# Kernel optimization log

Hardware: AMD Instinct MI355X
Metric: run time of the kernel (lower is better)

Reference implementation:

```python
import jax, jax.numpy as jnp
import numpy as np


def _greedy_nms_single(scores, suppress):
    """Greedy score-ordered suppression for one scene.
    scores: [P] float max class score; suppress: [P, P] bool, row i suppresses col j
    (same class AND within class radius of point i). Returns keep mask [P] bool."""
    P = scores.shape[0]

    def cond(state):
        alive, _ = state
        return jnp.any(alive)

    def body(state):
        alive, keep = state
        i = jnp.argmax(jnp.where(alive, scores, -jnp.inf))  # highest-score remaining
        keep = keep.at[i].set(True)
        alive = alive & ~suppress[i]   # drop same-class points within radius of i
        alive = alive.at[i].set(False)
        return alive, keep

    alive0 = jnp.ones((P,), dtype=bool)
    keep0 = jnp.zeros((P,), dtype=bool)
    _, keep = jax.lax.while_loop(cond, body, (alive0, keep0))
    return keep


def _keep_mask(centers, cls_preds, class_radius):
    # centers: [B,P,3], cls_preds: [B,P,K], class_radius: [K]
    scores = jnp.max(cls_preds, axis=-1)     # [B,P]  torch.max(..., dim=1) values
    labels = jnp.argmax(cls_preds, axis=-1)  # [B,P]  torch.max(..., dim=1) indices
    diff = centers[:, :, None, :] - centers[:, None, :, :]        # [B,P,P,3]
    dist = jnp.sqrt(jnp.sum(diff * diff, axis=-1))                # [B,P,P] torch.norm
    same_class = labels[:, :, None] == labels[:, None, :]         # [B,P,P]
    radii = class_radius[labels]                                  # [B,P] radius of keeper i
    suppress = same_class & (dist < radii[:, :, None])            # [B,P,P]
    return jax.vmap(_greedy_nms_single)(scores, suppress)         # [B,P] bool


def setup_inputs() -> dict:
    key = jax.random.key(0)
    k1, k2, k3, k4 = jax.random.split(key, 4)
    B, P, C, K = 8, 2048, 1024, 3
    centers = jax.random.normal(k1, (B, P, 3), dtype=jnp.float32)
    features = jax.random.normal(k2, (B, P, C), dtype=jnp.float32)
    cls_preds = jax.random.normal(k3, (B, P, K), dtype=jnp.float32)
    class_radius = jax.random.uniform(k4, (K,), dtype=jnp.float32)  # per-class NMS radius
    return {"centers": centers, "features": features, "cls_preds": cls_preds,
            "class_radius": class_radius}


def reference(centers, features, cls_preds, class_radius):
    """Greedy per-class radius-based keypoint suppression (fixed-shape variant):
    instead of dynamically gathering kept points (data-dependent shape), we return
    the boolean keep mask and the inputs with suppressed entries zeroed out."""
    keep = _keep_mask(centers, cls_preds, class_radius)      # [B,P] bool
    m = keep[..., None].astype(features.dtype)
    return (centers * m, features * m, cls_preds * m, keep)
```

## Files before the change

kernel.cpp:

```cpp
#include <hip/hip_runtime.h>

#define B 8
#define P 2048
#define C 1024
#define NCHUNK 32
#define FEAT4 (B*P*C/4)
#define CEN4  (B*P*3/4)

typedef unsigned long long u64;
typedef unsigned int u32;

__device__ __forceinline__ u64 shfl_xor_u64(u64 x, int m) {
    int lo = __shfl_xor((int)(u32)x, m, 64);
    int hi = __shfl_xor((int)(u32)(x >> 32), m, 64);
    return ((u64)(u32)hi << 32) | (u32)lo;
}

__global__ __launch_bounds__(1024) void sort_kernel(
    const float* __restrict__ centers,
    const float* __restrict__ cls_preds,
    float4* __restrict__ scent,
    int* __restrict__ sidx)
{
    __shared__ u64 s_k[P];
    const int b = blockIdx.x, tid = threadIdx.x;
    const float* clsb = cls_preds + (size_t)b * P * 3;
    const float* cenb = centers + (size_t)b * P * 3;

    u64 v[2];
    #pragma unroll
    for (int h = 0; h < 2; ++h) {
        int e = tid + h * 1024;
        float s0 = clsb[e*3], s1 = clsb[e*3+1], s2 = clsb[e*3+2];
        float sc = s0; int lb = 0;
        if (s1 > sc) { sc = s1; lb = 1; }
        if (s2 > sc) { sc = s2; lb = 2; }
        u32 ub = __float_as_uint(sc);
        u32 ord = (ub & 0x80000000u) ? ~ub : (ub | 0x80000000u);
        v[h] = ((u64)(~ord) << 32) | (u32)((e << 2) | lb);
    }
    for (int k = 2; k <= P; k <<= 1) {
        for (int j = k >> 1; j >= 64; j >>= 1) {
            s_k[tid] = v[0]; s_k[tid + 1024] = v[1];
            __syncthreads();
            #pragma unroll
            for (int h = 0; h < 2; ++h) {
                int e = tid + h * 1024;
                u64 p = s_k[e ^ j];
                bool asc = (e & k) == 0, upper = (e & j) != 0;
                u64 mn = v[h] < p ? v[h] : p, mx = v[h] < p ? p : v[h];
                v[h] = (asc != upper) ? mn : mx;
            }
            __syncthreads();
        }
        int jt = (k >> 1) < 32 ? (k >> 1) : 32;
        for (int j = jt; j >= 1; j >>= 1) {
            #pragma unroll
            for (int h = 0; h < 2; ++h) {
                int e = tid + h * 1024;
                u64 p = shfl_xor_u64(v[h], j);
                bool asc = (e & k) == 0, upper = (e & j) != 0;
                u64 mn = v[h] < p ? v[h] : p, mx = v[h] < p ? p : v[h];
                v[h] = (asc != upper) ? mn : mx;
            }
        }
    }
    s_k[tid] = v[0]; s_k[tid + 1024] = v[1];
    __syncthreads();
    #pragma unroll
    for (int h = 0; h < 2; ++h) {
        int pos = tid + h * 1024;
        u32 lo = (u32)s_k[pos];
        int orig = (int)(lo >> 2);
        float4 c;
        c.x = cenb[orig*3]; c.y = cenb[orig*3+1]; c.z = cenb[orig*3+2];
        c.w = __int_as_float((int)(lo & 3));
        scent[b * P + pos] = c;
        sidx[b * P + pos] = (int)lo;
    }
}

__global__ __launch_bounds__(512) void matrix_kernel(
    const float4* __restrict__ scent,
    const float* __restrict__ class_radius,
    u32* __restrict__ matT)
{
    __shared__ float4 s_cent[P];
    const int b = blockIdx.x >> 5, gi = blockIdx.x & 31;
    const int tid = threadIdx.x, wv = tid >> 6, lane = tid & 63;

    const float4 cj = scent[(size_t)b * P + (gi << 6) + lane];
    const int labj = __float_as_int(cj.w);
    const float r = class_radius[labj];
    const float r2 = r * r;

    for (int i = tid; i < P; i += 512) s_cent[i] = scent[(size_t)b * P + i];
    __syncthreads();

    for (int w = wv; w < 64; w += 8) {
        u32 acc = 0;
        #pragma unroll
        for (int u = 0; u < 32; ++u) {
            float4 ci = s_cent[(w << 5) + u];
            float dx = cj.x - ci.x, dy = cj.y - ci.y, dz = cj.z - ci.z;
            bool sup = (__float_as_int(ci.w) == labj)
                       && (dx*dx + dy*dy + dz*dz < r2);
            acc |= ((u32)sup) << u;
        }
        matT[((size_t)b * 64 + w) * P + (gi << 6) + lane] = acc;
    }
}

__global__ __launch_bounds__(576) void scan_kernel(
    const u32* __restrict__ matT,
    const int* __restrict__ sidx,
    float* __restrict__ out_keep)
{
    __shared__ u32 s_tile[2][64][65];
    __shared__ u32 s_removed[64];
    __shared__ int s_sidx[P];
    const int b = blockIdx.x;
    const int tid = threadIdx.x, wv = tid >> 6, lane = tid & 63;
    const u32* mb = matT + (size_t)b * 64 * P;

    for (int i = tid; i < P; i += 576) s_sidx[i] = sidx[(size_t)b * P + i];
    if (tid < 64) s_removed[tid] = 0;
    if (wv >= 1) {
        #pragma unroll
        for (int rr = 0; rr < 8; ++rr) {
            int w = ((wv - 1) << 3) + rr;
            s_tile[0][lane][w] = mb[(size_t)w * P + lane];
        }
    }
    __syncthreads();

    for (int g = 0; g < NCHUNK; ++g) {
        const int buf = g & 1;
        if (wv >= 1 && g + 1 < NCHUNK) {
            const int nb = (g + 1) << 6;
            #pragma unroll
            for (int rr = 0; rr < 8; ++rr) {
                int w = ((wv - 1) << 3) + rr;
                s_tile[buf ^ 1][lane][w] = mb[(size_t)w * P + nb + lane];
            }
        }
        if (wv == 0) {
            const int base = g << 6;
            u64 row = (u64)s_tile[buf][lane][2*g]
                    | ((u64)s_tile[buf][lane][2*g + 1] << 32);
            u64 rem = (u64)s_removed[2*g] | ((u64)s_removed[2*g + 1] << 32);
            u64 alive = ~rem;
            const u64 below = (1ull << lane) - 1ull;
            u64 keepm = 0;
            while (alive) {
                bool ok = ((alive >> lane) & 1ull) && ((row & alive & below) == 0ull);
                u64 newk = __ballot(ok);
                keepm |= newk;
                bool dead = (row & newk) != 0ull;
                u64 deadm = __ballot(dead);
                alive &= ~(newk | deadm);
            }
            int orig = s_sidx[base + lane] >> 2;
            out_keep[(size_t)b * P + orig] = ((keepm >> lane) & 1ull) ? 1.0f : 0.0f;
            u32 acc = 0;
            u64 m = keepm;
            while (m) {
                int q = (int)__ffsll((long long)m) - 1;
                acc |= s_tile[buf][q][lane];
                m &= m - 1ull;
            }
            s_removed[lane] |= acc;
        }
        __syncthreads();
    }
}

__global__ __launch_bounds__(256) void mask_kernel(
    const float* __restrict__ centers,
    const float* __restrict__ features,
    const float* __restrict__ cls_preds,
    const float* __restrict__ keep,
    float* __restrict__ out_centers,
    float* __restrict__ out_feat,
    float* __restrict__ out_cls)
{
    const int idx = blockIdx.x * 256 + threadIdx.x;
    if (idx < FEAT4) {
        const int row = idx >> 8;
        const float m = keep[row];
        float4 v = ((const float4*)features)[idx];
        v.x *= m; v.y *= m; v.z *= m; v.w *= m;
        ((float4*)out_feat)[idx] = v;
    } else if (idx < FEAT4 + CEN4) {
        const int q = idx - FEAT4;
        float4 v = ((const float4*)centers)[q];
        const int e = q * 4;
        v.x *= keep[(e    ) / 3]; v.y *= keep[(e + 1) / 3];
        v.z *= keep[(e + 2) / 3]; v.w *= keep[(e + 3) / 3];
        ((float4*)out_centers)[q] = v;
    } else if (idx < FEAT4 + 2 * CEN4) {
        const int q = idx - FEAT4 - CEN4;
        float4 v = ((const float4*)cls_preds)[q];
        const int e = q * 4;
        v.x *= keep[(e    ) / 3]; v.y *= keep[(e + 1) / 3];
        v.z *= keep[(e + 2) / 3]; v.w *= keep[(e + 3) / 3];
        ((float4*)out_cls)[q] = v;
    }
}

extern "C" void kernel_launch(void* const* d_in, const int* in_sizes, int n_in,
                              void* d_out, int out_size, void* d_ws, size_t ws_size,
                              hipStream_t stream) {
    const float* centers      = (const float*)d_in[0];
    const float* features     = (const float*)d_in[1];
    const float* cls_preds    = (const float*)d_in[2];
    const float* class_radius = (const float*)d_in[3];

    float* out = (float*)d_out;
    float* out_centers = out;
    float* out_feat    = out + (size_t)B * P * 3;
    float* out_cls     = out_feat + (size_t)B * P * C;
    float* out_keep    = out_cls + (size_t)B * P * 3;

    u32*    matT  = (u32*)out_feat;
    float4* scent = (float4*)(out_feat + 1048576);
    int*    sidx  = (int*)(out_feat + 1048576 + 65536);

    hipLaunchKernelGGL(sort_kernel, dim3(B), dim3(1024), 0, stream,
                       centers, cls_preds, scent, sidx);
    hipLaunchKernelGGL(matrix_kernel, dim3(B * 32), dim3(512), 0, stream,
                       scent, class_radius, matT);
    hipLaunchKernelGGL(scan_kernel, dim3(B), dim3(576), 0, stream,
                       matT, sidx, out_keep);
    hipLaunchKernelGGL(mask_kernel, dim3((FEAT4 + 2 * CEN4 + 255) / 256), dim3(256),
                       0, stream,
                       centers, features, cls_preds, out_keep,
                       out_centers, out_feat, out_cls);
}
```

Measured before the change: 191.9 us.

## Replace per-batch bitonic sort with parallel rank-counting sort across many blocks

Swaps the single-block-per-scene bitonic sort for a rank sort: each of 256 blocks rebuilds the full key array for its scene in shared memory and computes exact ranks for 64 keys by counting smaller keys, split across 8 waves. This spreads the sort over many more CUs and removes the long chain of barrier-separated bitonic stages. In exchange it does O(P^2) comparisons and recomputes keys redundantly in every block. Keys are unique because they embed the index, so ranks form a valid permutation.

```diff
diff --git a/kernel.cpp b/kernel.cpp
--- a/kernel.cpp
+++ b/kernel.cpp
@@ -10,73 +10,50 @@
 typedef unsigned long long u64;
 typedef unsigned int u32;
 
-__device__ __forceinline__ u64 shfl_xor_u64(u64 x, int m) {
-    int lo = __shfl_xor((int)(u32)x, m, 64);
-    int hi = __shfl_xor((int)(u32)(x >> 32), m, 64);
-    return ((u64)(u32)hi << 32) | (u32)lo;
-}
-
-__global__ __launch_bounds__(1024) void sort_kernel(
+__global__ __launch_bounds__(512) void rank_kernel(
     const float* __restrict__ centers,
     const float* __restrict__ cls_preds,
     float4* __restrict__ scent,
     int* __restrict__ sidx)
 {
-    __shared__ u64 s_k[P];
-    const int b = blockIdx.x, tid = threadIdx.x;
+    __shared__ u64 s_keys[P];
+    __shared__ u32 s_cnt[64][9];
+    const int b = blockIdx.x >> 5, gi = blockIdx.x & 31;
+    const int tid = threadIdx.x, wv = tid >> 6, lane = tid & 63;
     const float* clsb = cls_preds + (size_t)b * P * 3;
     const float* cenb = centers + (size_t)b * P * 3;
 
-    u64 v[2];
-    #pragma unroll
-    for (int h = 0; h < 2; ++h) {
-        int e = tid + h * 1024;
+    for (int e = tid; e < P; e += 512) {
         float s0 = clsb[e*3], s1 = clsb[e*3+1], s2 = clsb[e*3+2];
         float sc = s0; int lb = 0;
         if (s1 > sc) { sc = s1; lb = 1; }
         if (s2 > sc) { sc = s2; lb = 2; }
         u32 ub = __float_as_uint(sc);
         u32 ord = (ub & 0x80000000u) ? ~ub : (ub | 0x80000000u);
-        v[h] = ((u64)(~ord) << 32) | (u32)((e << 2) | lb);
-    }
-    for (int k = 2; k <= P; k <<= 1) {
-        for (int j = k >> 1; j >= 64; j >>= 1) {
-            s_k[tid] = v[0]; s_k[tid + 1024] = v[1];
-            __syncthreads();
-            #pragma unroll
-            for (int h = 0; h < 2; ++h) {
-                int e = tid + h * 1024;
-                u64 p = s_k[e ^ j];
-                bool asc = (e & k) == 0, upper = (e & j) != 0;
-                u64 mn = v[h] < p ? v[h] : p, mx = v[h] < p ? p : v[h];
-                v[h] = (asc != upper) ? mn : mx;
-            }
-            __syncthreads();
-        }
-        int jt = (k >> 1) < 32 ? (k >> 1) : 32;
-        for (int j = jt; j >= 1; j >>= 1) {
-            #pragma unroll
-            for (int h = 0; h < 2; ++h) {
-                int e = tid + h * 1024;
-                u64 p = shfl_xor_u64(v[h], j);
-                bool asc = (e & k) == 0, upper = (e & j) != 0;
-                u64 mn = v[h] < p ? v[h] : p, mx = v[h] < p ? p : v[h];
-                v[h] = (asc != upper) ? mn : mx;
-            }
-        }
-    }
-    s_k[tid] = v[0]; s_k[tid + 1024] = v[1];
-    __syncthreads();
-    #pragma unroll
-    for (int h = 0; h < 2; ++h) {
-        int pos = tid + h * 1024;
-        u32 lo = (u32)s_k[pos];
+        s_keys[e] = ((u64)(~ord) << 32) | (u32)((e << 2) | lb);
+    }
+    __syncthreads();
+
+    const u64 myk = s_keys[(gi << 6) + lane];
+    u32 c = 0;
+    const int sbase = wv << 8;
+    #pragma unroll 8
+    for (int u = 0; u < 256; ++u)
+        c += (s_keys[sbase + u] < myk) ? 1u : 0u;
+    s_cnt[lane][wv] = c;
+    __syncthreads();
+
+    if (wv == 0) {
+        u32 rank = 0;
+        #pragma unroll
+        for (int s = 0; s < 8; ++s) rank += s_cnt[lane][s];
+        u32 lo = (u32)myk;
         int orig = (int)(lo >> 2);
-        float4 c;
-        c.x = cenb[orig*3]; c.y = cenb[orig*3+1]; c.z = cenb[orig*3+2];
-        c.w = __int_as_float((int)(lo & 3));
-        scent[b * P + pos] = c;
-        sidx[b * P + pos] = (int)lo;
+        float4 cc;
+        cc.x = cenb[orig*3]; cc.y = cenb[orig*3+1]; cc.z = cenb[orig*3+2];
+        cc.w = __int_as_float((int)(lo & 3));
+        scent[(size_t)b * P + rank] = cc;
+        sidx[(size_t)b * P + rank] = (int)lo;
     }
 }
 
@@ -226,7 +203,7 @@
     float4* scent = (float4*)(out_feat + 1048576);
     int*    sidx  = (int*)(out_feat + 1048576 + 65536);
 
-    hipLaunchKernelGGL(sort_kernel, dim3(B), dim3(1024), 0, stream,
+    hipLaunchKernelGGL(rank_kernel, dim3(B * 32), dim3(512), 0, stream,
                        centers, cls_preds, scent, sidx);
     hipLaunchKernelGGL(matrix_kernel, dim3(B * 32), dim3(512), 0, stream,
                        scent, class_radius, matT);
```

Measured after the change: 180.1 us. 6.1% less time.
